# Kernel optimization log

Hardware: AMD Instinct MI355X
Metric: run time of the kernel (lower is better)

The kernel has to match this reference:

```python
import jax, jax.numpy as jnp
import numpy as np
import math

B, F, N, EMB, H, NC, L = 16, 60, 512, 128, 4, 27, 2
EPS = 1e-5


def _ln(x, g, b):
    m = x.mean(-1, keepdims=True)
    v = ((x - m) ** 2).mean(-1, keepdims=True)
    return (x - m) / jnp.sqrt(v + EPS) * g + b


def _bn(x, g, b):
    # BatchNorm1d in training mode: batch statistics over dim 0
    m = x.mean(0)
    v = ((x - m) ** 2).mean(0)
    return (x - m) / jnp.sqrt(v + EPS) * g + b


def _pos_encoding(S, D):
    pos = jnp.arange(S, dtype=jnp.float32)[:, None]
    div = jnp.exp(jnp.arange(0, D, 2, dtype=jnp.float32) * (-math.log(10000.0) / D))
    ang = pos * div  # [S, D/2]
    return jnp.stack([jnp.sin(ang), jnp.cos(ang)], axis=-1).reshape(S, D)


def setup_inputs():
    key = jax.random.key(0)
    ks = jax.random.split(key, 16)
    rn = lambda i, shape, s: (jax.random.normal(ks[i], shape) * s).astype(jnp.float32)
    z = lambda *shape: jnp.zeros(shape, jnp.float32)
    o = lambda *shape: jnp.ones(shape, jnp.float32)
    return {
        "x": jax.random.normal(ks[0], (B, F, N, 3), dtype=jnp.float32),
        "frame_length": jax.random.randint(ks[1], (B,), 1, F + 1, dtype=jnp.int32),
        # PointNet encoder (shared per-point MLP 3->64->128->EMB, max-pool)
        "enc_w1": rn(2, (3, 64), 0.3), "enc_b1": z(64),
        "enc_w2": rn(3, (64, 128), 0.1), "enc_b2": z(128),
        "enc_w3": rn(4, (128, EMB), 0.1), "enc_b3": z(EMB),
        "cls_token": rn(5, (1, 1, EMB), 0.02), "cls_pos": rn(6, (1, 1, EMB), 0.02),
        # 2-layer post-norm TransformerEncoder (d=128, h=4, ff=256)
        "in_w": rn(7, (L, 3 * EMB, EMB), 0.05), "in_b": z(L, 3 * EMB),
        "out_w": rn(8, (L, EMB, EMB), 0.05), "out_b": z(L, EMB),
        "ln1_g": o(L, EMB), "ln1_b": z(L, EMB),
        "ff1_w": rn(9, (L, 256, EMB), 0.05), "ff1_b": z(L, 256),
        "ff2_w": rn(10, (L, EMB, 256), 0.05), "ff2_b": z(L, EMB),
        "ln2_g": o(L, EMB), "ln2_b": z(L, EMB),
        # MLP head (weights stored [in, out])
        "fc1_w": rn(11, (2 * EMB, 128), 0.05), "fc1_b": z(128),
        "bn1_g": o(128), "bn1_b": z(128),
        "fc15_w": rn(12, (128, 64), 0.05), "fc15_b": z(64),
        "bn15_g": o(64), "bn15_b": z(64),
        "fc2_w": rn(13, (64, 32), 0.05), "fc2_b": z(32),
        "bn2_g": o(32), "bn2_b": z(32),
        "fc_w": rn(14, (32, NC), 0.05), "fc_b": z(NC),
    }


def _forward(x, frame_length, enc_w1, enc_b1, enc_w2, enc_b2, enc_w3, enc_b3,
             cls_token, cls_pos, in_w, in_b, out_w, out_b, ln1_g, ln1_b,
             ff1_w, ff1_b, ff2_w, ff2_b, ln2_g, ln2_b,
             fc1_w, fc1_b, bn1_g, bn1_b, fc15_w, fc15_b, bn15_g, bn15_b,
             fc2_w, fc2_b, bn2_g, bn2_b, fc_w, fc_b):
    dh = EMB // H
    # --- per-frame PointNet encoder, vectorized over (B, F) ---
    # (replaces the ragged Python loop; padded frames are masked to zero below,
    #  exactly matching y = zeros(...) filled only for valid frames)
    h = jax.nn.relu(jnp.einsum('bfnc,cd->bfnd', x, enc_w1) + enc_b1)
    h = jax.nn.relu(h @ enc_w2 + enc_b2)
    h = h @ enc_w3 + enc_b3
    y = h.max(axis=2)  # [B, F, EMB]
    valid = (jnp.arange(F)[None, :] < frame_length[:, None])  # [B, F]
    y = jnp.where(valid[..., None], y, 0.0)

    # --- cls token + sinusoidal positions ---
    pe = _pos_encoding(F, EMB)[None]  # [1, F, EMB]
    y = jnp.concatenate([jnp.broadcast_to(cls_token, (B, 1, EMB)), y], axis=1)
    pos = jnp.concatenate([cls_pos, pe], axis=1)
    y = y + pos  # [B, F+1, EMB]

    S = F + 1
    kpm = jnp.arange(S)[None, :] >= (frame_length + 1)[:, None]  # True = pad
    bias = jnp.where(kpm, -1e9, 0.0)[:, None, None, :]  # [B,1,1,S]

    for l in range(L):
        qkv = y @ in_w[l].T + in_b[l]  # [B,S,3*EMB]
        q, k, v = jnp.split(qkv, 3, axis=-1)
        q = q.reshape(B, S, H, dh).transpose(0, 2, 1, 3)
        k = k.reshape(B, S, H, dh).transpose(0, 2, 1, 3)
        v = v.reshape(B, S, H, dh).transpose(0, 2, 1, 3)
        scores = jnp.einsum('bhqd,bhkd->bhqk', q, k) / math.sqrt(dh) + bias
        attn = jax.nn.softmax(scores, axis=-1)
        o = jnp.einsum('bhqk,bhkd->bhqd', attn, v).transpose(0, 2, 1, 3).reshape(B, S, EMB)
        y = _ln(y + (o @ out_w[l].T + out_b[l]), ln1_g[l], ln1_b[l])
        ff = jax.nn.relu(y @ ff1_w[l].T + ff1_b[l]) @ ff2_w[l].T + ff2_b[l]
        y = _ln(y + ff, ln2_g[l], ln2_b[l])

    # --- ragged gather: cls output + last valid frame output ---
    z1 = y[:, 0, :]
    z2 = y[jnp.arange(B), frame_length]  # position frame_length[i] (cls offset)
    zc = jnp.concatenate([z1, z2], axis=1)  # [B, 2*EMB]

    lrelu = lambda t: jax.nn.leaky_relu(t, negative_slope=0.2)
    y1 = lrelu(_bn(zc @ fc1_w + fc1_b, bn1_g, bn1_b))
    y1 = lrelu(_bn(y1 @ fc15_w + fc15_b, bn15_g, bn15_b))
    y1 = lrelu(_bn(y1 @ fc2_w + fc2_b, bn2_g, bn2_b))
    return y1 @ fc_w + fc_b  # [B, NC]


def reference(x, frame_length, enc_w1, enc_b1, enc_w2, enc_b2, enc_w3, enc_b3,
              cls_token, cls_pos, in_w, in_b, out_w, out_b, ln1_g, ln1_b,
              ff1_w, ff1_b, ff2_w, ff2_b, ln2_g, ln2_b,
              fc1_w, fc1_b, bn1_g, bn1_b, fc15_w, fc15_b, bn15_g, bn15_b,
              fc2_w, fc2_b, bn2_g, bn2_b, fc_w, fc_b):
    return _forward(x, frame_length, enc_w1, enc_b1, enc_w2, enc_b2, enc_w3, enc_b3,
                    cls_token, cls_pos, in_w, in_b, out_w, out_b, ln1_g, ln1_b,
                    ff1_w, ff1_b, ff2_w, ff2_b, ln2_g, ln2_b,
                    fc1_w, fc1_b, bn1_g, bn1_b, fc15_w, fc15_b, bn15_g, bn15_b,
                    fc2_w, fc2_b, bn2_g, bn2_b, fc_w, fc_b)
```

## Files before the change

kernel.cpp:

```cpp
#include <hip/hip_runtime.h>
#include <math.h>

#define SS 61
#define EPSV 1e-5f

typedef __attribute__((ext_vector_type(8))) short bf16x8;
typedef __attribute__((ext_vector_type(4))) short s16x4;
typedef __attribute__((ext_vector_type(4))) float f32x4;

__device__ __forceinline__ short f2bf(float f){
  return __builtin_bit_cast(short, (__bf16)f);
}
__device__ __forceinline__ float bf2f(short s){
  unsigned u = ((unsigned)(unsigned short)s) << 16;
  return __builtin_bit_cast(float, u);
}
__device__ __forceinline__ bf16x8 pack8(f32x4 lo, f32x4 hi){
  bf16x8 r;
  r[0]=f2bf(lo[0]); r[1]=f2bf(lo[1]); r[2]=f2bf(lo[2]); r[3]=f2bf(lo[3]);
  r[4]=f2bf(hi[0]); r[5]=f2bf(hi[1]); r[6]=f2bf(hi[2]); r[7]=f2bf(hi[3]);
  return r;
}
__device__ __forceinline__ s16x4 pack4(f32x4 v){
  s16x4 r; r[0]=f2bf(v[0]); r[1]=f2bf(v[1]); r[2]=f2bf(v[2]); r[3]=f2bf(v[3]); return r;
}
#define YI(t,d) (((t)<<7) + ((d) ^ (((t)&7)<<2)))
#define OI(t,e) (((t)<<7) + ((e) ^ (((t)&7)<<2)))
#define FI(t,e) (((t)<<8) + ((e) ^ (((t)&7)<<2)))
#define VI(k,d) (((k)<<5) + ((d) ^ (((k)&7)<<2)))

__global__ __launch_bounds__(256) void prep_kernel(
    const float* __restrict__ ew1, const float* __restrict__ eb1,
    const float* __restrict__ ew2, const float* __restrict__ ew3,
    const float* __restrict__ in_w, const float* __restrict__ ow,
    const float* __restrict__ f1w, const float* __restrict__ f2w,
    const float* __restrict__ fc1w, const float* __restrict__ fc15w,
    const float* __restrict__ fc2w, const float* __restrict__ fcw,
    unsigned short* __restrict__ wbf)
{
  int s = blockIdx.x * 256 + threadIdx.x;
  int i = s & 7, lane = (s >> 3) & 63, frag = s >> 9;
  int c = lane & 15, g = lane >> 4;
  int sig = 16 * (i >> 2) + 4 * g + (i & 3);
  unsigned short outv;
  if (frag < 8) {
    int mt = frag & 3;
    float base = (sig < 3) ? ew1[sig * 64 + 16 * mt + c]
               : (sig == 3 ? eb1[16 * mt + c] : 0.f);
    short hv = f2bf(base);
    if (frag < 4) outv = (unsigned short)hv;
    else { float rv = base - bf2f(hv); outv = (unsigned short)f2bf(rv); }
  } else if (frag < 24) {
    int f = frag - 8; int mt = f >> 1, ks = f & 1;
    outv = (unsigned short)f2bf(ew2[(32 * ks + sig) * 128 + 16 * mt + c]);
  } else if (frag < 56) {
    int f = frag - 24; int mt = f >> 2, ks = f & 3;
    outv = (unsigned short)f2bf(ew3[(32 * ks + sig) * 128 + 16 * mt + c]);
  } else if (frag < 568) {
    int f = frag - 56; int l = f >> 8; f &= 255;
    float v;
    if (f < 96) { int tq = f >> 2, ks = f & 3;
      v = in_w[(size_t)l * 49152 + (size_t)(16 * tq + c) * 128 + 32 * ks + sig]; }
    else if (f < 128) { int f3 = f - 96; int t = f3 >> 2, ks = f3 & 3;
      v = ow[(size_t)l * 16384 + (size_t)(16 * t + c) * 128 + 32 * ks + sig]; }
    else if (f < 192) { int f3 = f - 128; int t = f3 >> 2, ks = f3 & 3;
      v = f1w[(size_t)l * 32768 + (size_t)(16 * t + c) * 128 + 32 * ks + sig]; }
    else { int f3 = f - 192; int t = f3 >> 3, ks = f3 & 7;
      v = f2w[(size_t)l * 32768 + (size_t)(16 * t + c) * 256 + 32 * ks + sig]; }
    outv = (unsigned short)f2bf(v);
  } else {
    int f = frag - 568;
    float v; int hl;
    if (f < 128) { hl = f >> 6; int f6 = f & 63; int mt = f6 >> 3, ks = f6 & 7;
      v = fc1w[(32 * ks + sig) * 128 + 16 * mt + c]; }
    else if (f < 160) { int f2_ = f - 128; hl = f2_ >> 4; int f4 = f2_ & 15; int mt = f4 >> 2, ks = f4 & 3;
      v = fc15w[(32 * ks + sig) * 64 + 16 * mt + c]; }
    else if (f < 168) { int f2_ = f - 160; hl = f2_ >> 2; int f4 = f2_ & 3; int mt = f4 >> 1, ks = f4 & 1;
      v = fc2w[(32 * ks + sig) * 32 + 16 * mt + c]; }
    else { int f2_ = f - 168; hl = f2_ >> 1; int mt = f2_ & 1; int m = 16 * mt + c;
      v = (m < 27) ? fcw[sig * 27 + m] : 0.f; }
    short hv = f2bf(v);
    outv = hl ? (unsigned short)f2bf(v - bf2f(hv)) : (unsigned short)hv;
  }
  wbf[s] = outv;
}

__global__ __launch_bounds__(256, 1) void enc_kernel(
    const float* __restrict__ x,
    const float* __restrict__ ew1, const float* __restrict__ eb1,
    const float* __restrict__ eb2, const float* __restrict__ eb3,
    const unsigned short* __restrict__ wbf,
    float* __restrict__ ymax)
{
  const int tid = threadIdx.x, lane = tid & 63, wv = tid >> 6;
  const int c = lane & 15, g = lane >> 4;
  const int frame = blockIdx.x * 4 + wv;
  const bf16x8* wf = (const bf16x8*)wbf;

  float wa[2][8], wb_[2][8], wc_[2][8], b1v[2][8];
#pragma unroll
  for (int ks = 0; ks < 2; ks++)
#pragma unroll
    for (int i = 0; i < 8; i++) {
      const int ch = 32 * ks + 16 * (i >> 2) + 4 * g + (i & 3);
      wa[ks][i]  = ew1[ch];
      wb_[ks][i] = ew1[64 + ch];
      wc_[ks][i] = ew1[128 + ch];
      b1v[ks][i] = eb1[ch];
    }

  bf16x8 A2f[8][2];
#pragma unroll
  for (int mt = 0; mt < 8; mt++)
#pragma unroll
    for (int ks = 0; ks < 2; ks++) A2f[mt][ks] = wf[(8 + mt * 2 + ks) * 64 + lane];
  bf16x8 A3f[8][4];
#pragma unroll
  for (int mt = 0; mt < 8; mt++)
#pragma unroll
    for (int ks = 0; ks < 4; ks++) A3f[mt][ks] = wf[(24 + mt * 4 + ks) * 64 + lane];
  f32x4 b2v[8];
#pragma unroll
  for (int mt = 0; mt < 8; mt++) b2v[mt] = *(const f32x4*)(eb2 + 16 * mt + 4 * g);

  f32x4 pool[8];
#pragma unroll
  for (int mt = 0; mt < 8; mt++) pool[mt] = {-1e30f, -1e30f, -1e30f, -1e30f};

  const float* xf = x + (size_t)frame * 1536;
  float nx[2][3];
#pragma unroll
  for (int nt = 0; nt < 2; nt++) {
    const float* xp = xf + (16 * nt + c) * 3;
    nx[nt][0] = xp[0]; nx[nt][1] = xp[1]; nx[nt][2] = xp[2];
  }

  for (int t = 0; t < 16; t++) {
    float cx[2][3];
#pragma unroll
    for (int nt = 0; nt < 2; nt++) {
      cx[nt][0] = nx[nt][0]; cx[nt][1] = nx[nt][1]; cx[nt][2] = nx[nt][2];
    }
    if (t < 15) {
#pragma unroll
      for (int nt = 0; nt < 2; nt++) {
        const float* xp = xf + ((t + 1) * 32 + 16 * nt + c) * 3;
        nx[nt][0] = xp[0]; nx[nt][1] = xp[1]; nx[nt][2] = xp[2];
      }
    }
#pragma unroll
    for (int nt = 0; nt < 2; nt++) {
      bf16x8 B2[2];
#pragma unroll
      for (int ks = 0; ks < 2; ks++) {
        bf16x8 r;
#pragma unroll
        for (int i = 0; i < 8; i++) {
          float h = fmaf(cx[nt][0], wa[ks][i],
                    fmaf(cx[nt][1], wb_[ks][i],
                    fmaf(cx[nt][2], wc_[ks][i], b1v[ks][i])));
          r[i] = f2bf(fmaxf(h, 0.f));
        }
        B2[ks] = r;
      }
      f32x4 acc2[8];
#pragma unroll
      for (int mt = 0; mt < 8; mt++) {
        f32x4 a = b2v[mt];
        a = __builtin_amdgcn_mfma_f32_16x16x32_bf16(A2f[mt][0], B2[0], a, 0, 0, 0);
        a = __builtin_amdgcn_mfma_f32_16x16x32_bf16(A2f[mt][1], B2[1], a, 0, 0, 0);
        acc2[mt] = a;
      }
      bf16x8 B3[4];
#pragma unroll
      for (int ks = 0; ks < 4; ks++) {
        bf16x8 r;
#pragma unroll
        for (int i = 0; i < 8; i++)
          r[i] = f2bf(fmaxf(acc2[2 * ks + (i >> 2)][i & 3], 0.f));
        B3[ks] = r;
      }
#pragma unroll
      for (int mt = 0; mt < 8; mt++) {
        f32x4 a = {0.f, 0.f, 0.f, 0.f};
        a = __builtin_amdgcn_mfma_f32_16x16x32_bf16(A3f[mt][0], B3[0], a, 0, 0, 0);
        a = __builtin_amdgcn_mfma_f32_16x16x32_bf16(A3f[mt][1], B3[1], a, 0, 0, 0);
        a = __builtin_amdgcn_mfma_f32_16x16x32_bf16(A3f[mt][2], B3[2], a, 0, 0, 0);
        a = __builtin_amdgcn_mfma_f32_16x16x32_bf16(A3f[mt][3], B3[3], a, 0, 0, 0);
#pragma unroll
        for (int r = 0; r < 4; r++) pool[mt][r] = fmaxf(pool[mt][r], a[r]);
      }
    }
  }

#pragma unroll
  for (int mt = 0; mt < 8; mt++)
#pragma unroll
    for (int r = 0; r < 4; r++) {
      float v = pool[mt][r];
      v = fmaxf(v, __shfl_xor(v, 1, 64));
      v = fmaxf(v, __shfl_xor(v, 2, 64));
      v = fmaxf(v, __shfl_xor(v, 4, 64));
      v = fmaxf(v, __shfl_xor(v, 8, 64));
      pool[mt][r] = v;
    }
  if (c == 0) {
#pragma unroll
    for (int mt = 0; mt < 8; mt++)
#pragma unroll
      for (int r = 0; r < 4; r++) {
        const int ch = 16 * mt + 4 * g + r;
        ymax[(size_t)frame * 128 + ch] = pool[mt][r] + eb3[ch];
      }
  }
}

__global__ __launch_bounds__(512, 1) void xformer_kernel(
    const float* __restrict__ ymax, const int* __restrict__ fl,
    const float* __restrict__ ctok, const float* __restrict__ cpos,
    const unsigned short* __restrict__ wbf,
    const float* __restrict__ in_b, const float* __restrict__ ob,
    const float* __restrict__ l1g, const float* __restrict__ l1b,
    const float* __restrict__ f1b, const float* __restrict__ f2b,
    const float* __restrict__ l2g, const float* __restrict__ l2b,
    float* __restrict__ zbuf)
{
  __shared__ __align__(16) float ylds[64 * 128];
  __shared__ __align__(16) unsigned short ubuf[64 * 256];
  __shared__ __align__(16) unsigned short kq4[2][8][4][64][4];
  const int b = blockIdx.x, tid = threadIdx.x;
  const int w8 = tid >> 6, lane = tid & 63, c = lane & 15, g = lane >> 4;
  const int h = w8 >> 1, sub = w8 & 1;
  const int flb = fl[b];
  const float scl = 0.17677669529663687f;

  for (int it = 0; it < 16; it++) {
    int idx = it * 512 + tid;
    int t = idx >> 7, d = idx & 127;
    float v;
    if (t == 0) v = ctok[d] + cpos[d];
    else if (t <= 60) {
      int f = t - 1;
      float ym = (f < flb) ? ymax[(size_t)(b * 60 + f) * 128 + d] : 0.f;
      float dv = __expf((float)(d & ~1) * (-0.07195578416f));
      float ang = (float)f * dv;
      v = ym + ((d & 1) ? __cosf(ang) : __sinf(ang));
    } else v = 0.f;
    ylds[YI(t, d)] = v;
  }
  __syncthreads();

  for (int l = 0; l < 2; l++) {
    const unsigned short* WL = wbf + 28672 + (size_t)l * 131072;
    const bf16x8* wq  = (const bf16x8*)WL;
    const bf16x8* wo  = (const bf16x8*)(WL + 49152);
    const bf16x8* w1p = (const bf16x8*)(WL + 65536);
    const bf16x8* w2p = (const bf16x8*)(WL + 98304);
    unsigned short* vb = ubuf + 8192 + h * 2048;

    {
      bf16x8 yB[4][4];
#pragma unroll
      for (int nt = 0; nt < 4; nt++)
#pragma unroll
        for (int ks = 0; ks < 4; ks++) {
          f32x4 lo = *(const f32x4*)&ylds[YI(16 * nt + c, 32 * ks + 4 * g)];
          f32x4 hi = *(const f32x4*)&ylds[YI(16 * nt + c, 32 * ks + 16 + 4 * g)];
          yB[nt][ks] = pack8(lo, hi);
        }
#pragma unroll
      for (int p = 0; p < 3; p++) {
        const int tq = p * 8 + w8;
        bf16x8 Af[4];
#pragma unroll
        for (int ks = 0; ks < 4; ks++) Af[ks] = wq[(tq * 4 + ks) * 64 + lane];
        f32x4 bias = *(const f32x4*)(in_b + l * 384 + p * 128 + 16 * w8 + 4 * g);
        f32x4 acc[4];
#pragma unroll
        for (int nt = 0; nt < 4; nt++) acc[nt] = bias;
#pragma unroll
        for (int ks = 0; ks < 4; ks++)
#pragma unroll
          for (int nt = 0; nt < 4; nt++)
            acc[nt] = __builtin_amdgcn_mfma_f32_16x16x32_bf16(Af[ks], yB[nt][ks], acc[nt], 0, 0, 0);
        if (p == 2) {
#pragma unroll
          for (int nt = 0; nt < 4; nt++)
            *(s16x4*)&vb[VI(16 * nt + c, 16 * sub + 4 * g)] = pack4(acc[nt]);
        } else {
#pragma unroll
          for (int nt = 0; nt < 4; nt++) {
            f32x4 sv = acc[nt];
            if (p == 0) sv = sv * scl;
            *(s16x4*)&kq4[p][w8][nt][lane][0] = pack4(sv);
          }
        }
      }
    }
    __syncthreads();

    {
      bf16x8 Ak[4], Bq2[2];
#pragma unroll
      for (int kt = 0; kt < 4; kt++) {
        s16x4 lo = *(const s16x4*)&kq4[1][2 * h][kt][lane][0];
        s16x4 hi = *(const s16x4*)&kq4[1][2 * h + 1][kt][lane][0];
        Ak[kt] = __builtin_shufflevector(lo, hi, 0, 1, 2, 3, 4, 5, 6, 7);
      }
#pragma unroll
      for (int j = 0; j < 2; j++) {
        s16x4 lo = *(const s16x4*)&kq4[0][2 * h][2 * sub + j][lane][0];
        s16x4 hi = *(const s16x4*)&kq4[0][2 * h + 1][2 * sub + j][lane][0];
        Bq2[j] = __builtin_shufflevector(lo, hi, 0, 1, 2, 3, 4, 5, 6, 7);
      }
      f32x4 St[4][2];
#pragma unroll
      for (int kt = 0; kt < 4; kt++)
#pragma unroll
        for (int j = 0; j < 2; j++) {
          f32x4 z = {0.f, 0.f, 0.f, 0.f};
          St[kt][j] = __builtin_amdgcn_mfma_f32_16x16x32_bf16(Ak[kt], Bq2[j], z, 0, 0, 0);
        }
#pragma unroll
      for (int j = 0; j < 2; j++) {
        float m = -1e30f;
#pragma unroll
        for (int kt = 0; kt < 4; kt++)
#pragma unroll
          for (int r = 0; r < 4; r++) {
            const int kp = 16 * kt + 4 * g + r;
            float s = St[kt][j][r];
            s = (kp > flb) ? -1e30f : s;
            St[kt][j][r] = s;
            m = fmaxf(m, s);
          }
        m = fmaxf(m, __shfl_xor(m, 16, 64));
        m = fmaxf(m, __shfl_xor(m, 32, 64));
        float sum = 0.f;
#pragma unroll
        for (int kt = 0; kt < 4; kt++)
#pragma unroll
          for (int r = 0; r < 4; r++) {
            float p = __expf(St[kt][j][r] - m);
            St[kt][j][r] = p;
            sum += p;
          }
        sum += __shfl_xor(sum, 16, 64);
        sum += __shfl_xor(sum, 32, 64);
        const float inv = 1.f / sum;
#pragma unroll
        for (int kt = 0; kt < 4; kt++)
#pragma unroll
          for (int r = 0; r < 4; r++) St[kt][j][r] *= inv;
      }
      bf16x8 Bp[2][2];
#pragma unroll
      for (int j = 0; j < 2; j++)
#pragma unroll
        for (int ks = 0; ks < 2; ks++) {
          bf16x8 r;
#pragma unroll
          for (int i = 0; i < 8; i++) r[i] = f2bf(St[2 * ks + (i >> 2)][j][i & 3]);
          Bp[j][ks] = r;
        }
      bf16x8 Av[2][2];
#pragma unroll
      for (int dt = 0; dt < 2; dt++)
#pragma unroll
        for (int ks = 0; ks < 2; ks++) {
          bf16x8 r;
#pragma unroll
          for (int i = 0; i < 8; i++) {
            const int kp = 32 * ks + 16 * (i >> 2) + 4 * g + (i & 3);
            r[i] = (short)vb[VI(kp, 16 * dt + c)];
          }
          Av[dt][ks] = r;
        }
#pragma unroll
      for (int dt = 0; dt < 2; dt++)
#pragma unroll
        for (int j = 0; j < 2; j++) {
          f32x4 z = {0.f, 0.f, 0.f, 0.f};
          z = __builtin_amdgcn_mfma_f32_16x16x32_bf16(Av[dt][0], Bp[j][0], z, 0, 0, 0);
          z = __builtin_amdgcn_mfma_f32_16x16x32_bf16(Av[dt][1], Bp[j][1], z, 0, 0, 0);
          *(s16x4*)&ubuf[OI(16 * (2 * sub + j) + c, 32 * h + 16 * dt + 4 * g)] = pack4(z);
        }
    }
    __syncthreads();

    {
      bf16x8 Bo[4][4];
#pragma unroll
      for (int nt = 0; nt < 4; nt++)
#pragma unroll
        for (int ks = 0; ks < 4; ks++) {
          s16x4 lo = *(const s16x4*)&ubuf[OI(16 * nt + c, 32 * ks + 4 * g)];
          s16x4 hi = *(const s16x4*)&ubuf[OI(16 * nt + c, 32 * ks + 16 + 4 * g)];
          Bo[nt][ks] = __builtin_shufflevector(lo, hi, 0, 1, 2, 3, 4, 5, 6, 7);
        }
      const int j0 = 16 * w8;
      bf16x8 Af[4];
#pragma unroll
      for (int ks = 0; ks < 4; ks++) Af[ks] = wo[(w8 * 4 + ks) * 64 + lane];
      f32x4 bias = *(const f32x4*)(ob + l * 128 + j0 + 4 * g);
      f32x4 acc[4];
#pragma unroll
      for (int nt = 0; nt < 4; nt++) acc[nt] = bias;
#pragma unroll
      for (int ks = 0; ks < 4; ks++)
#pragma unroll
        for (int nt = 0; nt < 4; nt++)
          acc[nt] = __builtin_amdgcn_mfma_f32_16x16x32_bf16(Af[ks], Bo[nt][ks], acc[nt], 0, 0, 0);
#pragma unroll
      for (int nt = 0; nt < 4; nt++) {
        float* yp = &ylds[YI(16 * nt + c, j0 + 4 * g)];
        *(f32x4*)yp = *(const f32x4*)yp + acc[nt];
      }
    }
    __syncthreads();
    {
      const int t = 8 * w8 + (lane >> 3);
      const int s = lane & 7;
      f32x4 vv[4];
      float s1 = 0.f, s2 = 0.f;
#pragma unroll
      for (int k = 0; k < 4; k++) {
        vv[k] = *(const f32x4*)&ylds[YI(t, s * 16 + 4 * k)];
#pragma unroll
        for (int r = 0; r < 4; r++) { s1 += vv[k][r]; s2 = fmaf(vv[k][r], vv[k][r], s2); }
      }
      s1 += __shfl_xor(s1, 1, 64); s1 += __shfl_xor(s1, 2, 64); s1 += __shfl_xor(s1, 4, 64);
      s2 += __shfl_xor(s2, 1, 64); s2 += __shfl_xor(s2, 2, 64); s2 += __shfl_xor(s2, 4, 64);
      const float mean = s1 * 0.0078125f;
      const float var  = s2 * 0.0078125f - mean * mean;
      const float inv  = rsqrtf(var + EPSV);
#pragma unroll
      for (int k = 0; k < 4; k++) {
        f32x4 gg = *(const f32x4*)(l1g + l * 128 + s * 16 + 4 * k);
        f32x4 bb = *(const f32x4*)(l1b + l * 128 + s * 16 + 4 * k);
        f32x4 o;
#pragma unroll
        for (int r = 0; r < 4; r++) o[r] = (vv[k][r] - mean) * inv * gg[r] + bb[r];
        *(f32x4*)&ylds[YI(t, s * 16 + 4 * k)] = o;
      }
    }
    __syncthreads();

    {
      bf16x8 yB[4][4];
#pragma unroll
      for (int nt = 0; nt < 4; nt++)
#pragma unroll
        for (int ks = 0; ks < 4; ks++) {
          f32x4 lo = *(const f32x4*)&ylds[YI(16 * nt + c, 32 * ks + 4 * g)];
          f32x4 hi = *(const f32x4*)&ylds[YI(16 * nt + c, 32 * ks + 16 + 4 * g)];
          yB[nt][ks] = pack8(lo, hi);
        }
#pragma unroll
      for (int half = 0; half < 2; half++) {
        const int t16 = 8 * half + w8;
        bf16x8 Af[4];
#pragma unroll
        for (int ks = 0; ks < 4; ks++) Af[ks] = w1p[(t16 * 4 + ks) * 64 + lane];
        f32x4 bias = *(const f32x4*)(f1b + l * 256 + 16 * t16 + 4 * g);
        f32x4 acc[4];
#pragma unroll
        for (int nt = 0; nt < 4; nt++) acc[nt] = bias;
#pragma unroll
        for (int ks = 0; ks < 4; ks++)
#pragma unroll
          for (int nt = 0; nt < 4; nt++)
            acc[nt] = __builtin_amdgcn_mfma_f32_16x16x32_bf16(Af[ks], yB[nt][ks], acc[nt], 0, 0, 0);
#pragma unroll
        for (int nt = 0; nt < 4; nt++) {
          f32x4 rl;
#pragma unroll
          for (int r = 0; r < 4; r++) rl[r] = fmaxf(acc[nt][r], 0.f);
          *(s16x4*)&ubuf[FI(16 * nt + c, 16 * t16 + 4 * g)] = pack4(rl);
        }
      }
    }
    __syncthreads();
    {
      f32x4 acc[4];
      f32x4 bias = *(const f32x4*)(f2b + l * 128 + 16 * w8 + 4 * g);
#pragma unroll
      for (int nt = 0; nt < 4; nt++) acc[nt] = bias;
#pragma unroll
      for (int ks = 0; ks < 8; ks++) {
        bf16x8 Af = w2p[(w8 * 8 + ks) * 64 + lane];
        bf16x8 Bf[4];
#pragma unroll
        for (int nt = 0; nt < 4; nt++) {
          s16x4 lo = *(const s16x4*)&ubuf[FI(16 * nt + c, 32 * ks + 4 * g)];
          s16x4 hi = *(const s16x4*)&ubuf[FI(16 * nt + c, 32 * ks + 16 + 4 * g)];
          Bf[nt] = __builtin_shufflevector(lo, hi, 0, 1, 2, 3, 4, 5, 6, 7);
        }
#pragma unroll
        for (int nt = 0; nt < 4; nt++)
          acc[nt] = __builtin_amdgcn_mfma_f32_16x16x32_bf16(Af, Bf[nt], acc[nt], 0, 0, 0);
      }
#pragma unroll
      for (int nt = 0; nt < 4; nt++) {
        float* yp = &ylds[YI(16 * nt + c, 16 * w8 + 4 * g)];
        *(f32x4*)yp = *(const f32x4*)yp + acc[nt];
      }
    }
    __syncthreads();
    {
      const int t = 8 * w8 + (lane >> 3);
      const int s = lane & 7;
      f32x4 vv[4];
      float s1 = 0.f, s2 = 0.f;
#pragma unroll
      for (int k = 0; k < 4; k++) {
        vv[k] = *(const f32x4*)&ylds[YI(t, s * 16 + 4 * k)];
#pragma unroll
        for (int r = 0; r < 4; r++) { s1 += vv[k][r]; s2 = fmaf(vv[k][r], vv[k][r], s2); }
      }
      s1 += __shfl_xor(s1, 1, 64); s1 += __shfl_xor(s1, 2, 64); s1 += __shfl_xor(s1, 4, 64);
      s2 += __shfl_xor(s2, 1, 64); s2 += __shfl_xor(s2, 2, 64); s2 += __shfl_xor(s2, 4, 64);
      const float mean = s1 * 0.0078125f;
      const float var  = s2 * 0.0078125f - mean * mean;
      const float inv  = rsqrtf(var + EPSV);
#pragma unroll
      for (int k = 0; k < 4; k++) {
        f32x4 gg = *(const f32x4*)(l2g + l * 128 + s * 16 + 4 * k);
        f32x4 bb = *(const f32x4*)(l2b + l * 128 + s * 16 + 4 * k);
        f32x4 o;
#pragma unroll
        for (int r = 0; r < 4; r++) o[r] = (vv[k][r] - mean) * inv * gg[r] + bb[r];
        *(f32x4*)&ylds[YI(t, s * 16 + 4 * k)] = o;
      }
    }
    __syncthreads();
  }

  if (tid < 256) {
    const int d = tid;
    float v = (d < 128) ? ylds[YI(0, d)] : ylds[YI(flb, d - 128)];
    zbuf[d * 16 + b] = v;
  }
}

__device__ __forceinline__ void buildB(const float* src, int ks, int g, int c,
                                       bf16x8& bh, bf16x8& bl){
#pragma unroll
  for (int i = 0; i < 8; i++) {
    int k = 32 * ks + 16 * (i >> 2) + 4 * g + (i & 3);
    float v = src[k * 16 + c];
    short hv = f2bf(v);
    bh[i] = hv; bl[i] = f2bf(v - bf2f(hv));
  }
}
__device__ __forceinline__ void bn_lrelu_store(f32x4 acc, int ch0, int c,
    const float* __restrict__ gg, const float* __restrict__ bb, float* dst){
#pragma unroll
  for (int r = 0; r < 4; r++) {
    float v = acc[r];
    float s1 = v, s2 = v * v;
    s1 += __shfl_xor(s1, 1, 64); s2 += __shfl_xor(s2, 1, 64);
    s1 += __shfl_xor(s1, 2, 64); s2 += __shfl_xor(s2, 2, 64);
    s1 += __shfl_xor(s1, 4, 64); s2 += __shfl_xor(s2, 4, 64);
    s1 += __shfl_xor(s1, 8, 64); s2 += __shfl_xor(s2, 8, 64);
    const float m = s1 * (1.f / 16.f);
    const float var = s2 * (1.f / 16.f) - m * m;
    const float scl = gg[ch0 + r] / sqrtf(var + EPSV);
    const float sh = bb[ch0 + r] - m * scl;
    float o = v * scl + sh;
    o = (o > 0.f) ? o : 0.2f * o;
    dst[(ch0 + r) * 16 + c] = o;
  }
}

__global__ __launch_bounds__(256, 1) void head_kernel(
    const float* __restrict__ zt, const unsigned short* __restrict__ wbf,
    const float* __restrict__ fc1b, const float* __restrict__ bn1g, const float* __restrict__ bn1b,
    const float* __restrict__ fc15b, const float* __restrict__ bn15g, const float* __restrict__ bn15b,
    const float* __restrict__ fc2b, const float* __restrict__ bn2g, const float* __restrict__ bn2b,
    const float* __restrict__ fcb, float* __restrict__ out)
{
  __shared__ float zs[256 * 16];
  __shared__ float t1s[128 * 16];
  __shared__ float t15s[64 * 16];
  __shared__ float t2s[32 * 16];
  const int tid = threadIdx.x, lane = tid & 63, wv = tid >> 6;
  const int c = lane & 15, g = lane >> 4;
  const bf16x8* wf = (const bf16x8*)wbf;

  for (int idx = tid; idx < 4096; idx += 256) zs[idx] = zt[idx];
  __syncthreads();

  {
    f32x4 acc[2];
#pragma unroll
    for (int j = 0; j < 2; j++) {
      const int ch0 = 16 * (2 * wv + j) + 4 * g;
      f32x4 a;
#pragma unroll
      for (int r = 0; r < 4; r++) a[r] = fc1b[ch0 + r];
      acc[j] = a;
    }
#pragma unroll
    for (int ks = 0; ks < 8; ks++) {
      bf16x8 bh, bl; buildB(zs, ks, g, c, bh, bl);
#pragma unroll
      for (int j = 0; j < 2; j++) {
        const int mt = 2 * wv + j;
        bf16x8 Ah = wf[(568 + mt * 8 + ks) * 64 + lane];
        bf16x8 Al = wf[(632 + mt * 8 + ks) * 64 + lane];
        acc[j] = __builtin_amdgcn_mfma_f32_16x16x32_bf16(Ah, bh, acc[j], 0, 0, 0);
        acc[j] = __builtin_amdgcn_mfma_f32_16x16x32_bf16(Ah, bl, acc[j], 0, 0, 0);
        acc[j] = __builtin_amdgcn_mfma_f32_16x16x32_bf16(Al, bh, acc[j], 0, 0, 0);
      }
    }
#pragma unroll
    for (int j = 0; j < 2; j++)
      bn_lrelu_store(acc[j], 16 * (2 * wv + j) + 4 * g, c, bn1g, bn1b, t1s);
  }
  __syncthreads();

  {
    const int ch0 = 16 * wv + 4 * g;
    f32x4 a;
#pragma unroll
    for (int r = 0; r < 4; r++) a[r] = fc15b[ch0 + r];
#pragma unroll
    for (int ks = 0; ks < 4; ks++) {
      bf16x8 bh, bl; buildB(t1s, ks, g, c, bh, bl);
      bf16x8 Ah = wf[(696 + wv * 4 + ks) * 64 + lane];
      bf16x8 Al = wf[(712 + wv * 4 + ks) * 64 + lane];
      a = __builtin_amdgcn_mfma_f32_16x16x32_bf16(Ah, bh, a, 0, 0, 0);
      a = __builtin_amdgcn_mfma_f32_16x16x32_bf16(Ah, bl, a, 0, 0, 0);
      a = __builtin_amdgcn_mfma_f32_16x16x32_bf16(Al, bh, a, 0, 0, 0);
    }
    bn_lrelu_store(a, ch0, c, bn15g, bn15b, t15s);
  }
  __syncthreads();

  if (wv < 2) {
    const int ch0 = 16 * wv + 4 * g;
    f32x4 a;
#pragma unroll
    for (int r = 0; r < 4; r++) a[r] = fc2b[ch0 + r];
#pragma unroll
    for (int ks = 0; ks < 2; ks++) {
      bf16x8 bh, bl; buildB(t15s, ks, g, c, bh, bl);
      bf16x8 Ah = wf[(728 + wv * 2 + ks) * 64 + lane];
      bf16x8 Al = wf[(732 + wv * 2 + ks) * 64 + lane];
      a = __builtin_amdgcn_mfma_f32_16x16x32_bf16(Ah, bh, a, 0, 0, 0);
      a = __builtin_amdgcn_mfma_f32_16x16x32_bf16(Ah, bl, a, 0, 0, 0);
      a = __builtin_amdgcn_mfma_f32_16x16x32_bf16(Al, bh, a, 0, 0, 0);
    }
    bn_lrelu_store(a, ch0, c, bn2g, bn2b, t2s);
  }
  __syncthreads();

  if (wv < 2) {
    f32x4 a;
#pragma unroll
    for (int r = 0; r < 4; r++) {
      const int ch = 16 * wv + 4 * g + r;
      a[r] = (ch < 27) ? fcb[ch] : 0.f;
    }
    bf16x8 bh, bl; buildB(t2s, 0, g, c, bh, bl);
    bf16x8 Ah = wf[(736 + wv) * 64 + lane];
    bf16x8 Al = wf[(738 + wv) * 64 + lane];
    a = __builtin_amdgcn_mfma_f32_16x16x32_bf16(Ah, bh, a, 0, 0, 0);
    a = __builtin_amdgcn_mfma_f32_16x16x32_bf16(Ah, bl, a, 0, 0, 0);
    a = __builtin_amdgcn_mfma_f32_16x16x32_bf16(Al, bh, a, 0, 0, 0);
#pragma unroll
    for (int r = 0; r < 4; r++) {
      const int ch = 16 * wv + 4 * g + r;
      if (ch < 27) out[c * 27 + ch] = a[r];
    }
  }
}

extern "C" void kernel_launch(void* const* d_in, const int* in_sizes, int n_in,
                              void* d_out, int out_size, void* d_ws, size_t ws_size,
                              hipStream_t stream)
{
  const float* x    = (const float*)d_in[0];
  const int*   fl   = (const int*)d_in[1];
  const float* ew1  = (const float*)d_in[2];  const float* eb1 = (const float*)d_in[3];
  const float* ew2  = (const float*)d_in[4];  const float* eb2 = (const float*)d_in[5];
  const float* ew3  = (const float*)d_in[6];  const float* eb3 = (const float*)d_in[7];
  const float* ctok = (const float*)d_in[8];  const float* cpos = (const float*)d_in[9];
  const float* in_w = (const float*)d_in[10]; const float* in_b = (const float*)d_in[11];
  const float* ow   = (const float*)d_in[12]; const float* ob   = (const float*)d_in[13];
  const float* l1g  = (const float*)d_in[14]; const float* l1b  = (const float*)d_in[15];
  const float* f1w  = (const float*)d_in[16]; const float* f1b  = (const float*)d_in[17];
  const float* f2w  = (const float*)d_in[18]; const float* f2b  = (const float*)d_in[19];
  const float* l2g  = (const float*)d_in[20]; const float* l2b  = (const float*)d_in[21];
  const float* fc1w = (const float*)d_in[22]; const float* fc1b = (const float*)d_in[23];
  const float* bn1g = (const float*)d_in[24]; const float* bn1b = (const float*)d_in[25];
  const float* fc15w= (const float*)d_in[26]; const float* fc15b= (const float*)d_in[27];
  const float* bn15g= (const float*)d_in[28]; const float* bn15b= (const float*)d_in[29];
  const float* fc2w = (const float*)d_in[30]; const float* fc2b = (const float*)d_in[31];
  const float* bn2g = (const float*)d_in[32]; const float* bn2b = (const float*)d_in[33];
  const float* fcw  = (const float*)d_in[34]; const float* fcb  = (const float*)d_in[35];
  float* out = (float*)d_out;

  char* w = (char*)d_ws;
  float* ymax = (float*)w;
  float* zbuf = (float*)(w + 491520);
  unsigned short* wbf = (unsigned short*)(w + 507904);

  prep_kernel<<<1480, 256, 0, stream>>>(ew1, eb1, ew2, ew3, in_w, ow, f1w, f2w,
                                        fc1w, fc15w, fc2w, fcw, wbf);
  enc_kernel<<<240, 256, 0, stream>>>(x, ew1, eb1, eb2, eb3, wbf, ymax);
  xformer_kernel<<<16, 512, 0, stream>>>(ymax, fl, ctok, cpos, wbf, in_b, ob,
                                         l1g, l1b, f1b, f2b, l2g, l2b, zbuf);
  head_kernel<<<1, 256, 0, stream>>>(zbuf, wbf, fc1b, bn1g, bn1b,
                                     fc15b, bn15g, bn15b, fc2b, bn2g, bn2b, fcb, out);
}
```

Baseline: 77.89 us.

## Split encoder frames across two waves and stage MLP weights in LDS

The encoder now launches 512 threads per block: two waves share each frame, each handling half of the points. Their partial max-pools are merged through shared memory and written out coalesced. Layer-2/3 MFMA weights move from per-lane registers into LDS and are read per tile, and the layer-1 weights are packed as bf16 pairs, which lowers register pressure so two blocks can fit per CU. The goal is more active waves to hide MFMA and load latency, at the cost of repeated LDS reads, an extra barrier, and bf16 rounding of the first-layer weights and biases.

```diff
diff --git a/kernel.cpp b/kernel.cpp
--- a/kernel.cpp
+++ b/kernel.cpp
@@ -85,40 +85,41 @@
   wbf[s] = outv;
 }
 
-__global__ __launch_bounds__(256, 1) void enc_kernel(
+__global__ __launch_bounds__(512, 2) void enc_kernel(
     const float* __restrict__ x,
     const float* __restrict__ ew1, const float* __restrict__ eb1,
     const float* __restrict__ eb2, const float* __restrict__ eb3,
     const unsigned short* __restrict__ wbf,
     float* __restrict__ ymax)
 {
+  __shared__ __align__(16) unsigned short wlds[48 * 512];
+  __shared__ float pmerge[4][2][128];
   const int tid = threadIdx.x, lane = tid & 63, wv = tid >> 6;
   const int c = lane & 15, g = lane >> 4;
-  const int frame = blockIdx.x * 4 + wv;
-  const bf16x8* wf = (const bf16x8*)wbf;
-
-  float wa[2][8], wb_[2][8], wc_[2][8], b1v[2][8];
+  const int fl_ = wv >> 1, half = wv & 1;
+  const int frame = blockIdx.x * 4 + fl_;
+
+  {
+    const bf16x8* wsrc = (const bf16x8*)wbf;
+    bf16x8* wdst = (bf16x8*)wlds;
+#pragma unroll
+    for (int i = 0; i < 6; i++) wdst[i * 512 + tid] = wsrc[512 + i * 512 + tid];
+  }
+
+  unsigned wpa[2][4], wpb[2][4], wpc[2][4], wpd[2][4];
 #pragma unroll
   for (int ks = 0; ks < 2; ks++)
 #pragma unroll
-    for (int i = 0; i < 8; i++) {
-      const int ch = 32 * ks + 16 * (i >> 2) + 4 * g + (i & 3);
-      wa[ks][i]  = ew1[ch];
-      wb_[ks][i] = ew1[64 + ch];
-      wc_[ks][i] = ew1[128 + ch];
-      b1v[ks][i] = eb1[ch];
-    }
-
-  bf16x8 A2f[8][2];
-#pragma unroll
-  for (int mt = 0; mt < 8; mt++)
-#pragma unroll
-    for (int ks = 0; ks < 2; ks++) A2f[mt][ks] = wf[(8 + mt * 2 + ks) * 64 + lane];
-  bf16x8 A3f[8][4];
-#pragma unroll
-  for (int mt = 0; mt < 8; mt++)
-#pragma unroll
-    for (int ks = 0; ks < 4; ks++) A3f[mt][ks] = wf[(24 + mt * 4 + ks) * 64 + lane];
+    for (int j = 0; j < 4; j++) {
+      const int i0 = 2 * j, i1 = 2 * j + 1;
+      const int ch0 = 32 * ks + 16 * (i0 >> 2) + 4 * g + (i0 & 3);
+      const int ch1 = 32 * ks + 16 * (i1 >> 2) + 4 * g + (i1 & 3);
+      wpa[ks][j] = (unsigned)(unsigned short)f2bf(ew1[ch0])        | ((unsigned)(unsigned short)f2bf(ew1[ch1]) << 16);
+      wpb[ks][j] = (unsigned)(unsigned short)f2bf(ew1[64 + ch0])   | ((unsigned)(unsigned short)f2bf(ew1[64 + ch1]) << 16);
+      wpc[ks][j] = (unsigned)(unsigned short)f2bf(ew1[128 + ch0])  | ((unsigned)(unsigned short)f2bf(ew1[128 + ch1]) << 16);
+      wpd[ks][j] = (unsigned)(unsigned short)f2bf(eb1[ch0])        | ((unsigned)(unsigned short)f2bf(eb1[ch1]) << 16);
+    }
+
   f32x4 b2v[8];
 #pragma unroll
   for (int mt = 0; mt < 8; mt++) b2v[mt] = *(const f32x4*)(eb2 + 16 * mt + 4 * g);
@@ -128,65 +129,77 @@
   for (int mt = 0; mt < 8; mt++) pool[mt] = {-1e30f, -1e30f, -1e30f, -1e30f};
 
   const float* xf = x + (size_t)frame * 1536;
-  float nx[2][3];
-#pragma unroll
-  for (int nt = 0; nt < 2; nt++) {
-    const float* xp = xf + (16 * nt + c) * 3;
-    nx[nt][0] = xp[0]; nx[nt][1] = xp[1]; nx[nt][2] = xp[2];
-  }
-
-  for (int t = 0; t < 16; t++) {
+  const bf16x8* wl = (const bf16x8*)wlds;
+  __syncthreads();
+
+  for (int tt = 0; tt < 8; tt++) {
+    const int t = 8 * half + tt;
     float cx[2][3];
 #pragma unroll
     for (int nt = 0; nt < 2; nt++) {
-      cx[nt][0] = nx[nt][0]; cx[nt][1] = nx[nt][1]; cx[nt][2] = nx[nt][2];
-    }
-    if (t < 15) {
-#pragma unroll
-      for (int nt = 0; nt < 2; nt++) {
-        const float* xp = xf + ((t + 1) * 32 + 16 * nt + c) * 3;
-        nx[nt][0] = xp[0]; nx[nt][1] = xp[1]; nx[nt][2] = xp[2];
-      }
-    }
-#pragma unroll
-    for (int nt = 0; nt < 2; nt++) {
-      bf16x8 B2[2];
+      const float* xp = xf + (t * 32 + 16 * nt + c) * 3;
+      cx[nt][0] = xp[0]; cx[nt][1] = xp[1]; cx[nt][2] = xp[2];
+    }
+    bf16x8 B2[2][2];
+#pragma unroll
+    for (int nt = 0; nt < 2; nt++)
 #pragma unroll
       for (int ks = 0; ks < 2; ks++) {
         bf16x8 r;
 #pragma unroll
-        for (int i = 0; i < 8; i++) {
-          float h = fmaf(cx[nt][0], wa[ks][i],
-                    fmaf(cx[nt][1], wb_[ks][i],
-                    fmaf(cx[nt][2], wc_[ks][i], b1v[ks][i])));
-          r[i] = f2bf(fmaxf(h, 0.f));
-        }
-        B2[ks] = r;
-      }
-      f32x4 acc2[8];
-#pragma unroll
-      for (int mt = 0; mt < 8; mt++) {
+        for (int j = 0; j < 4; j++) {
+          const float a0 = __builtin_bit_cast(float, wpa[ks][j] << 16);
+          const float a1 = __builtin_bit_cast(float, wpa[ks][j] & 0xffff0000u);
+          const float b0 = __builtin_bit_cast(float, wpb[ks][j] << 16);
+          const float b1 = __builtin_bit_cast(float, wpb[ks][j] & 0xffff0000u);
+          const float c0 = __builtin_bit_cast(float, wpc[ks][j] << 16);
+          const float c1 = __builtin_bit_cast(float, wpc[ks][j] & 0xffff0000u);
+          const float d0 = __builtin_bit_cast(float, wpd[ks][j] << 16);
+          const float d1 = __builtin_bit_cast(float, wpd[ks][j] & 0xffff0000u);
+          float h0 = fmaf(cx[nt][0], a0, fmaf(cx[nt][1], b0, fmaf(cx[nt][2], c0, d0)));
+          float h1 = fmaf(cx[nt][0], a1, fmaf(cx[nt][1], b1, fmaf(cx[nt][2], c1, d1)));
+          r[2 * j]     = f2bf(fmaxf(h0, 0.f));
+          r[2 * j + 1] = f2bf(fmaxf(h1, 0.f));
+        }
+        B2[nt][ks] = r;
+      }
+    f32x4 acc2[8][2];
+#pragma unroll
+    for (int mt = 0; mt < 8; mt++) {
+      bf16x8 a0 = wl[(mt * 2 + 0) * 64 + lane];
+      bf16x8 a1 = wl[(mt * 2 + 1) * 64 + lane];
+#pragma unroll
+      for (int nt = 0; nt < 2; nt++) {
         f32x4 a = b2v[mt];
-        a = __builtin_amdgcn_mfma_f32_16x16x32_bf16(A2f[mt][0], B2[0], a, 0, 0, 0);
-        a = __builtin_amdgcn_mfma_f32_16x16x32_bf16(A2f[mt][1], B2[1], a, 0, 0, 0);
-        acc2[mt] = a;
-      }
-      bf16x8 B3[4];
+        a = __builtin_amdgcn_mfma_f32_16x16x32_bf16(a0, B2[nt][0], a, 0, 0, 0);
+        a = __builtin_amdgcn_mfma_f32_16x16x32_bf16(a1, B2[nt][1], a, 0, 0, 0);
+        acc2[mt][nt] = a;
+      }
+    }
+    bf16x8 B3[2][4];
+#pragma unroll
+    for (int nt = 0; nt < 2; nt++)
 #pragma unroll
       for (int ks = 0; ks < 4; ks++) {
         bf16x8 r;
 #pragma unroll
         for (int i = 0; i < 8; i++)
-          r[i] = f2bf(fmaxf(acc2[2 * ks + (i >> 2)][i & 3], 0.f));
-        B3[ks] = r;
-      }
-#pragma unroll
-      for (int mt = 0; mt < 8; mt++) {
+          r[i] = f2bf(fmaxf(acc2[2 * ks + (i >> 2)][nt][i & 3], 0.f));
+        B3[nt][ks] = r;
+      }
+#pragma unroll
+    for (int mt = 0; mt < 8; mt++) {
+      bf16x8 a3_0 = wl[(16 + mt * 4 + 0) * 64 + lane];
+      bf16x8 a3_1 = wl[(16 + mt * 4 + 1) * 64 + lane];
+      bf16x8 a3_2 = wl[(16 + mt * 4 + 2) * 64 + lane];
+      bf16x8 a3_3 = wl[(16 + mt * 4 + 3) * 64 + lane];
+#pragma unroll
+      for (int nt = 0; nt < 2; nt++) {
         f32x4 a = {0.f, 0.f, 0.f, 0.f};
-        a = __builtin_amdgcn_mfma_f32_16x16x32_bf16(A3f[mt][0], B3[0], a, 0, 0, 0);
-        a = __builtin_amdgcn_mfma_f32_16x16x32_bf16(A3f[mt][1], B3[1], a, 0, 0, 0);
-        a = __builtin_amdgcn_mfma_f32_16x16x32_bf16(A3f[mt][2], B3[2], a, 0, 0, 0);
-        a = __builtin_amdgcn_mfma_f32_16x16x32_bf16(A3f[mt][3], B3[3], a, 0, 0, 0);
+        a = __builtin_amdgcn_mfma_f32_16x16x32_bf16(a3_0, B3[nt][0], a, 0, 0, 0);
+        a = __builtin_amdgcn_mfma_f32_16x16x32_bf16(a3_1, B3[nt][1], a, 0, 0, 0);
+        a = __builtin_amdgcn_mfma_f32_16x16x32_bf16(a3_2, B3[nt][2], a, 0, 0, 0);
+        a = __builtin_amdgcn_mfma_f32_16x16x32_bf16(a3_3, B3[nt][3], a, 0, 0, 0);
 #pragma unroll
         for (int r = 0; r < 4; r++) pool[mt][r] = fmaxf(pool[mt][r], a[r]);
       }
@@ -207,11 +220,13 @@
   if (c == 0) {
 #pragma unroll
     for (int mt = 0; mt < 8; mt++)
-#pragma unroll
-      for (int r = 0; r < 4; r++) {
-        const int ch = 16 * mt + 4 * g + r;
-        ymax[(size_t)frame * 128 + ch] = pool[mt][r] + eb3[ch];
-      }
+      *(f32x4*)&pmerge[fl_][half][16 * mt + 4 * g] = pool[mt];
+  }
+  __syncthreads();
+  {
+    const int fr2 = tid >> 7, ch = tid & 127;
+    ymax[(size_t)(blockIdx.x * 4 + fr2) * 128 + ch] =
+        fmaxf(pmerge[fr2][0][ch], pmerge[fr2][1][ch]) + eb3[ch];
   }
 }
 
@@ -709,7 +724,7 @@
 
   prep_kernel<<<1480, 256, 0, stream>>>(ew1, eb1, ew2, ew3, in_w, ow, f1w, f2w,
                                         fc1w, fc15w, fc2w, fcw, wbf);
-  enc_kernel<<<240, 256, 0, stream>>>(x, ew1, eb1, eb2, eb3, wbf, ymax);
+  enc_kernel<<<240, 512, 0, stream>>>(x, ew1, eb1, eb2, eb3, wbf, ymax);
   xformer_kernel<<<16, 512, 0, stream>>>(ymax, fl, ctok, cpos, wbf, in_b, ob,
                                          l1g, l1b, f1b, f2b, l2g, l2b, zbuf);
   head_kernel<<<1, 256, 0, stream>>>(zbuf, wbf, fc1b, bn1g, bn1b,
```

After: 146.9 us. 1.89x slower.
